# Kernel tuning notes

Measured on AMD Instinct MI355X. Metric: run time of the kernel, lower is better.

The kernel has to match this reference:

```python
import jax, jax.numpy as jnp
import numpy as np

L = 8      # number of history layers backsubstituted (history[2:] in the torch code)
D = 2048   # layer width


def setup_inputs() -> dict:
    key = jax.random.key(0)
    ks = jax.random.split(key, 8)
    lower = jax.random.normal(ks[6], (D,), dtype=jnp.float32)
    upper = lower + jax.random.uniform(ks[7], (D,), dtype=jnp.float32)  # ensure lower <= upper
    return {
        "A": jax.random.normal(ks[0], (D, D), dtype=jnp.float32) * 0.05,
        "b": jax.random.normal(ks[1], (D,), dtype=jnp.float32) * 0.05,
        "hist_Al": jax.random.normal(ks[2], (L, D, D), dtype=jnp.float32) * 0.05,
        "hist_Au": jax.random.normal(ks[3], (L, D, D), dtype=jnp.float32) * 0.05,
        "hist_bl": jax.random.normal(ks[4], (L, D), dtype=jnp.float32) * 0.05,
        "hist_bu": jax.random.normal(ks[5], (L, D), dtype=jnp.float32) * 0.05,
        "lower_in": lower,
        "upper_in": upper,
    }


def reference(A, b, hist_Al, hist_Au, hist_bl, hist_bu, lower_in, upper_in):
    # Affine layer sets Al = Au = A, bl = bu = b, then backsubstitutes
    # through the history in reverse order (torch loop: i = len-1 .. 2).
    def step(carry, dp):
        Al, Au, bl, bu = carry
        dAl, dAu, dbl, dbu = dp
        Al_pos = jnp.maximum(Al, 0.0)
        Al_neg = jnp.minimum(Al, 0.0)
        Au_pos = jnp.maximum(Au, 0.0)
        Au_neg = jnp.minimum(Au, 0.0)
        new_Al = Al_pos @ dAl + Al_neg @ dAu
        new_bl = Al_pos @ dbl + Al_neg @ dbu + bl
        new_Au = Au_pos @ dAu + Au_neg @ dAl
        new_bu = Au_pos @ dbu + Au_neg @ dbl + bu
        return (new_Al, new_Au, new_bl, new_bu), None

    init = (A, A, b, b)
    # reverse the history so scan walks from the last layer back to the first
    dps = (hist_Al[::-1], hist_Au[::-1], hist_bl[::-1], hist_bu[::-1])
    (Al, Au, bl, bu), _ = jax.lax.scan(step, init, dps)

    # final concretization against the input box (history[1] in the torch code)
    lower = jnp.maximum(Al, 0.0) @ lower_in + jnp.minimum(Al, 0.0) @ upper_in + bl
    upper = jnp.maximum(Au, 0.0) @ upper_in + jnp.minimum(Au, 0.0) @ lower_in + bu
    return lower, upper
```

## Files before the change

kernel.cpp:

```cpp
#include <hip/hip_runtime.h>
#include <cstdint>
#include <cstddef>

#define D 2048
#define L 8
#define KT 4096
#define BM 256
#define BN 128
#define BK 32
#define NT (KT / BK)
#define BUFSZ ((BM + BN) * BK)

typedef _Float16 f16;
typedef _Float16 f16x4 __attribute__((ext_vector_type(4)));
typedef _Float16 f16x8 __attribute__((ext_vector_type(8)));
typedef float f32x4 __attribute__((ext_vector_type(4)));

__device__ __forceinline__ void gload16(const void* g, void* l) {
  __builtin_amdgcn_global_load_lds(
      (const __attribute__((address_space(1))) void*)g,
      (__attribute__((address_space(3))) void*)l, 16, 0, 0);
}

__global__ __launch_bounds__(256) void k_init(
    const float* __restrict__ A, const float* __restrict__ b,
    const float* __restrict__ db1, const float* __restrict__ db2,
    f16* __restrict__ Ab, float* __restrict__ blbu, float* __restrict__ outacc) {
  const int m = blockIdx.x, tid = threadIdx.x;
  if (m < 2) {
    f32x4 z = {0.f, 0.f, 0.f, 0.f};
    *(f32x4*)(outacc + m * 2048 + tid * 8) = z;
    *(f32x4*)(outacc + m * 2048 + tid * 8 + 4) = z;
  }
  const int k = tid * 8;
  size_t i = (size_t)m * D + k;
  f32x4 a0 = *(const f32x4*)(A + i);
  f32x4 a1 = *(const f32x4*)(A + i + 4);
  f16x8 p, n;
  float cL = 0.f, cU = 0.f;
#pragma unroll
  for (int j = 0; j < 8; ++j) {
    float v = (j < 4) ? a0[j] : a1[j - 4];
    float pf = fmaxf(v, 0.f), nf = fminf(v, 0.f);
    p[j] = (f16)pf; n[j] = (f16)nf;
    float w1 = db1[k + j], w2 = db2[k + j];
    cL += pf * w1 + nf * w2;
    cU += pf * w2 + nf * w1;
  }
  size_t lo = (size_t)m * KT + k;
  size_t hi = (size_t)(D + m) * KT + k;
  *(f16x8*)(Ab + lo) = p;      *(f16x8*)(Ab + lo + D) = n;
  *(f16x8*)(Ab + hi) = n;      *(f16x8*)(Ab + hi + D) = p;

  __shared__ float redL[4], redU[4];
#pragma unroll
  for (int off = 32; off > 0; off >>= 1) {
    cL += __shfl_down(cL, off);
    cU += __shfl_down(cU, off);
  }
  const int wave = tid >> 6, lane = tid & 63;
  if (lane == 0) { redL[wave] = cL; redU[wave] = cU; }
  __syncthreads();
  if (tid == 0) {
    float bL = b[m] + redL[0] + redL[1] + redL[2] + redL[3];
    float bU = b[m] + redU[0] + redU[1] + redU[2] + redU[3];
    blbu[m] = bL; blbu[D + m] = bU;
  }
}

__device__ __forceinline__ void transpose_panel(
    const float* __restrict__ srcAl, const float* __restrict__ srcAu,
    f16* __restrict__ Bb, int blk, int tid) {
  const int z = blk >> 10;
  const int rem = blk & 1023;
  const float* src = z ? srcAu : srcAl;
  const int koff = z ? D : 0;
  const int nb = (rem & 31) * 64;
  const int kb = (rem >> 5) * 64;
  const int col = nb + (tid & 63);
  const int k0 = kb + (tid >> 6) * 16;
  float v[16];
#pragma unroll
  for (int j = 0; j < 16; ++j)
    v[j] = src[(size_t)(k0 + j) * D + col];
  f16x8 h0, h1;
#pragma unroll
  for (int j = 0; j < 8; ++j) { h0[j] = (f16)v[j]; h1[j] = (f16)v[8 + j]; }
  f16* dst = Bb + (size_t)col * KT + koff + k0;
  *(f16x8*)dst = h0;
  *(f16x8*)(dst + 8) = h1;
}

__global__ __launch_bounds__(256) void k_prep(
    const float* __restrict__ srcAl, const float* __restrict__ srcAu,
    f16* __restrict__ Bb) {
  transpose_panel(srcAl, srcAu, Bb, blockIdx.x, threadIdx.x);
}

__global__ __launch_bounds__(256, 2) void k_gemm(
    const f16* __restrict__ A,
    const f16* __restrict__ BT,
    f16* __restrict__ BTn,
    const float* __restrict__ nAl, const float* __restrict__ nAu,
    const float* __restrict__ w1, const float* __restrict__ w2,
    float* __restrict__ bdst,
    f16* __restrict__ An) {
  __shared__ __align__(16) f16 lds[3 * BUFSZ];

  if (blockIdx.x >= 256) {
    transpose_panel(nAl, nAu, BTn, blockIdx.x - 256, threadIdx.x);
    return;
  }

  const int flat = blockIdx.x;
  const int xcd = flat & 7, idx = flat >> 3;
  const int by = (xcd >> 1) * 4 + (idx >> 3);
  const int bx = (xcd & 1) * 8 + (idx & 7);
  const int m0 = by * BM;
  const int n0 = bx * BN;

  const int tid = threadIdx.x;
  const int wave = tid >> 6, lane = tid & 63;
  const int wm = (wave >> 1) * 128, wn = (wave & 1) * 64;
  const int lr = lane & 15, lq = lane >> 4;
  const int srow = lane >> 2;
  const int scol = ((lane & 3) ^ ((lane >> 3) & 3)) * 8;
  const int rchunk = (lq ^ ((lr >> 1) & 3)) * 8;

  f32x4 acc[8][4];
#pragma unroll
  for (int m = 0; m < 8; ++m)
#pragma unroll
    for (int n = 0; n < 4; ++n)
      acc[m][n] = (f32x4){0.f, 0.f, 0.f, 0.f};

  auto stage = [&](int kt, int buf) {
    f16* bA = lds + buf * BUFSZ;
    f16* bB = bA + BM * BK;
    const size_t gk = (size_t)kt * BK;
#pragma unroll
    for (int i = 0; i < 4; ++i) {
      const int r = i * 4 + wave;
      gload16(A + (size_t)(m0 + r * 16 + srow) * KT + gk + scol, bA + r * 512);
    }
#pragma unroll
    for (int i = 0; i < 2; ++i) {
      const int r = i * 4 + wave;
      gload16(BT + (size_t)(n0 + r * 16 + srow) * KT + gk + scol, bB + r * 512);
    }
  };

  stage(0, 0);
  stage(1, 1);
  asm volatile("s_waitcnt vmcnt(6)" ::: "memory");
  __builtin_amdgcn_sched_barrier(0);
  __builtin_amdgcn_s_barrier();
  __builtin_amdgcn_sched_barrier(0);

  for (int t = 0; t < NT; ++t) {
    const f16* bA = lds + (t % 3) * BUFSZ;
    const f16* bB = bA + BM * BK;
    if (t + 2 < NT) stage(t + 2, (t + 2) % 3);
    f16x8 af[8], bf[4];
#pragma unroll
    for (int m = 0; m < 8; ++m)
      af[m] = *(const f16x8*)(bA + (wm + m * 16 + lr) * BK + rchunk);
#pragma unroll
    for (int n = 0; n < 4; ++n)
      bf[n] = *(const f16x8*)(bB + (wn + n * 16 + lr) * BK + rchunk);
    __builtin_amdgcn_s_setprio(1);
#pragma unroll
    for (int m = 0; m < 8; ++m)
#pragma unroll
      for (int n = 0; n < 4; ++n)
        acc[m][n] = __builtin_amdgcn_mfma_f32_16x16x32_f16(
            bf[n], af[m], acc[m][n], 0, 0, 0);
    __builtin_amdgcn_s_setprio(0);
    if (t + 2 < NT) {
      asm volatile("s_waitcnt vmcnt(6)" ::: "memory");
    } else if (t + 1 < NT) {
      asm volatile("s_waitcnt vmcnt(0)" ::: "memory");
    }
    __builtin_amdgcn_sched_barrier(0);
    __builtin_amdgcn_s_barrier();
    __builtin_amdgcn_sched_barrier(0);
  }

  const int low = (m0 < D) ? 1 : 0;
  f32x4 w1v[4], w2v[4];
#pragma unroll
  for (int n = 0; n < 4; ++n) {
    const int col = n0 + wn + n * 16 + lq * 4;
    w1v[n] = *(const f32x4*)(w1 + col);
    w2v[n] = *(const f32x4*)(w2 + col);
  }
  float rowsum[8] = {0.f, 0.f, 0.f, 0.f, 0.f, 0.f, 0.f, 0.f};
#pragma unroll
  for (int m = 0; m < 8; ++m) {
#pragma unroll
    for (int n = 0; n < 4; ++n) {
      const size_t row = (size_t)(m0 + wm + m * 16 + lr);
      const int col = n0 + wn + n * 16 + lq * 4;
      f16x4 p, q;
#pragma unroll
      for (int r = 0; r < 4; ++r) {
        float v = acc[m][n][r];
        float pf = fmaxf(v, 0.f), qf = fminf(v, 0.f);
        p[r] = (f16)pf;
        q[r] = (f16)qf;
        float wa = low ? w1v[n][r] : w2v[n][r];
        float wb = low ? w2v[n][r] : w1v[n][r];
        rowsum[m] += pf * wa + qf * wb;
      }
      f16* base = An + row * KT + col;
      if (low) { *(f16x4*)base = p; *(f16x4*)(base + D) = q; }
      else     { *(f16x4*)base = q; *(f16x4*)(base + D) = p; }
    }
  }
#pragma unroll
  for (int m = 0; m < 8; ++m) {
    float v = rowsum[m];
    v += __shfl_down(v, 32);
    v += __shfl_down(v, 16);
    if (lane < 16)
      atomicAdd(bdst + m0 + wm + m * 16 + lane, v);
  }
}

__global__ __launch_bounds__(256) void k_final(
    const float* __restrict__ outacc, const float* __restrict__ blbu,
    float* __restrict__ out) {
  const int R = blockIdx.x * 256 + threadIdx.x;
  out[R] = outacc[R] + blbu[R];
}

extern "C" void kernel_launch(void* const* d_in, const int* in_sizes, int n_in,
                              void* d_out, int out_size, void* d_ws, size_t ws_size,
                              hipStream_t stream) {
  (void)in_sizes; (void)n_in; (void)out_size;
  const float* A   = (const float*)d_in[0];
  const float* b   = (const float*)d_in[1];
  const float* hAl = (const float*)d_in[2];
  const float* hAu = (const float*)d_in[3];
  const float* hbl = (const float*)d_in[4];
  const float* hbu = (const float*)d_in[5];
  const float* lo  = (const float*)d_in[6];
  const float* up  = (const float*)d_in[7];
  float* out = (float*)d_out;

  const size_t AS = (size_t)2 * D * KT;
  const size_t BS = (size_t)D * KT;
  const size_t MS = (size_t)D * D;
  char* base = (char*)d_ws;
  f16* Ab0   = (f16*)base;
  f16* Ab1   = Ab0 + AS;
  f16* Bb0   = Ab1 + AS;
  float* blbu   = (float*)(Bb0 + BS);
  float* outacc = blbu + 2 * D;
  f16* Bb1   = (f16*)(outacc + 2 * D);
  const size_t need_fused = (size_t)((char*)(Bb1 + BS) - base);
  const bool fused = ws_size >= need_fused;

  k_init<<<dim3(D), 256, 0, stream>>>(
      A, b, hbl + (size_t)7 * D, hbu + (size_t)7 * D, Ab0, blbu, outacc);
  k_prep<<<dim3(2048), 256, 0, stream>>>(
      hAl + (size_t)7 * MS, hAu + (size_t)7 * MS, Bb0);

  f16* cur = Ab0;
  f16* nxt = Ab1;
  for (int t = 0; t < L; ++t) {
    const int nlayer = 6 - t;
    const float* w1 = (t < 7) ? hbl + (size_t)nlayer * D : lo;
    const float* w2 = (t < 7) ? hbu + (size_t)nlayer * D : up;
    float* bd = (t < 7) ? blbu : outacc;
    f16* BT  = (fused && (t & 1)) ? Bb1 : Bb0;
    f16* BTn = fused ? ((t & 1) ? Bb0 : Bb1) : Bb0;
    const float* nl = (t < 7) ? hAl + (size_t)nlayer * MS : hAl;
    const float* nu = (t < 7) ? hAu + (size_t)nlayer * MS : hAu;
    if (!fused && t > 0)
      k_prep<<<dim3(2048), 256, 0, stream>>>(
          hAl + (size_t)(7 - t) * MS, hAu + (size_t)(7 - t) * MS, Bb0);
    const unsigned grid = (fused && t < 7) ? 2304u : 256u;
    k_gemm<<<dim3(grid), 256, 0, stream>>>(cur, BT, BTn, nl, nu, w1, w2, bd, nxt);
    f16* tmp = cur; cur = nxt; nxt = tmp;
  }
  k_final<<<dim3(2 * D / 256), 256, 0, stream>>>(outacc, blbu, out);
}
```

Measured before the change: 726.8 us.

## Use 8 waves per GEMM block with ping-pong interleaved loads and MFMA

Doubles the GEMM block to 512 threads (8 waves), so each wave owns a 64x64 tile instead of 128x64, which halves the per-wave accumulator registers. The K-step is split into two halves, each with its own barrier, so that LDS reads and global prefetch issue overlap with MFMA bursts from other waves. The transpose panel is rewritten for 512 threads, each handling 8 k-values. This risks more barrier overhead and lower occupancy per CU because of the larger blocks.

```diff
diff --git a/kernel.cpp b/kernel.cpp
--- a/kernel.cpp
+++ b/kernel.cpp
@@ -78,26 +78,24 @@
   const int nb = (rem & 31) * 64;
   const int kb = (rem >> 5) * 64;
   const int col = nb + (tid & 63);
-  const int k0 = kb + (tid >> 6) * 16;
-  float v[16];
-#pragma unroll
-  for (int j = 0; j < 16; ++j)
+  const int k0 = kb + (tid >> 6) * 8;
+  float v[8];
+#pragma unroll
+  for (int j = 0; j < 8; ++j)
     v[j] = src[(size_t)(k0 + j) * D + col];
-  f16x8 h0, h1;
-#pragma unroll
-  for (int j = 0; j < 8; ++j) { h0[j] = (f16)v[j]; h1[j] = (f16)v[8 + j]; }
-  f16* dst = Bb + (size_t)col * KT + koff + k0;
-  *(f16x8*)dst = h0;
-  *(f16x8*)(dst + 8) = h1;
-}
-
-__global__ __launch_bounds__(256) void k_prep(
+  f16x8 h;
+#pragma unroll
+  for (int j = 0; j < 8; ++j) h[j] = (f16)v[j];
+  *(f16x8*)(Bb + (size_t)col * KT + koff + k0) = h;
+}
+
+__global__ __launch_bounds__(512) void k_prep(
     const float* __restrict__ srcAl, const float* __restrict__ srcAu,
     f16* __restrict__ Bb) {
   transpose_panel(srcAl, srcAu, Bb, blockIdx.x, threadIdx.x);
 }
 
-__global__ __launch_bounds__(256, 2) void k_gemm(
+__global__ __launch_bounds__(512, 2) void k_gemm(
     const f16* __restrict__ A,
     const f16* __restrict__ BT,
     f16* __restrict__ BTn,
@@ -121,38 +119,47 @@
 
   const int tid = threadIdx.x;
   const int wave = tid >> 6, lane = tid & 63;
-  const int wm = (wave >> 1) * 128, wn = (wave & 1) * 64;
+  const int wm = (wave & 3) * 64, wn = (wave >> 2) * 64;
   const int lr = lane & 15, lq = lane >> 4;
   const int srow = lane >> 2;
   const int scol = ((lane & 3) ^ ((lane >> 3) & 3)) * 8;
   const int rchunk = (lq ^ ((lr >> 1) & 3)) * 8;
 
-  f32x4 acc[8][4];
-#pragma unroll
-  for (int m = 0; m < 8; ++m)
+  f32x4 acc[4][4];
+#pragma unroll
+  for (int m = 0; m < 4; ++m)
 #pragma unroll
     for (int n = 0; n < 4; ++n)
       acc[m][n] = (f32x4){0.f, 0.f, 0.f, 0.f};
 
-  auto stage = [&](int kt, int buf) {
-    f16* bA = lds + buf * BUFSZ;
-    f16* bB = bA + BM * BK;
-    const size_t gk = (size_t)kt * BK;
-#pragma unroll
-    for (int i = 0; i < 4; ++i) {
-      const int r = i * 4 + wave;
-      gload16(A + (size_t)(m0 + r * 16 + srow) * KT + gk + scol, bA + r * 512);
-    }
-#pragma unroll
-    for (int i = 0; i < 2; ++i) {
-      const int r = i * 4 + wave;
-      gload16(BT + (size_t)(n0 + r * 16 + srow) * KT + gk + scol, bB + r * 512);
-    }
+  auto stageA = [&](size_t gk, f16* sA, int i) {
+    const int r = i * 8 + wave;
+    gload16(A + (size_t)(m0 + r * 16 + srow) * KT + gk + scol, sA + r * 512);
   };
-
-  stage(0, 0);
-  stage(1, 1);
-  asm volatile("s_waitcnt vmcnt(6)" ::: "memory");
+  auto stageB = [&](size_t gk, f16* sB) {
+    gload16(BT + (size_t)(n0 + wave * 16 + srow) * KT + gk + scol,
+            sB + wave * 512);
+  };
+  auto lda = [&](const f16* bA, int m) {
+    return *(const f16x8*)(bA + (wm + m * 16 + lr) * BK + rchunk);
+  };
+  auto ldb = [&](const f16* bB, int n) {
+    return *(const f16x8*)(bB + (wn + n * 16 + lr) * BK + rchunk);
+  };
+
+#define SYNC_PRE()  do { __builtin_amdgcn_sched_barrier(0);                 \
+    __builtin_amdgcn_s_barrier();                                           \
+    asm volatile("s_waitcnt lgkmcnt(0)" ::: "memory");                      \
+    __builtin_amdgcn_sched_barrier(0); } while (0)
+#define SYNC_POST() do { __builtin_amdgcn_sched_barrier(0);                 \
+    __builtin_amdgcn_s_barrier(); } while (0)
+
+  { f16* s0 = lds;            f16* s0b = s0 + BM * BK;
+    f16* s1 = lds + BUFSZ;    f16* s1b = s1 + BM * BK;
+    stageA(0, s0, 0); stageA(0, s0, 1); stageB(0, s0b);
+    stageA(BK, s1, 0); stageA(BK, s1, 1); stageB(BK, s1b);
+  }
+  asm volatile("s_waitcnt vmcnt(3)" ::: "memory");
   __builtin_amdgcn_sched_barrier(0);
   __builtin_amdgcn_s_barrier();
   __builtin_amdgcn_sched_barrier(0);
@@ -160,30 +167,46 @@
   for (int t = 0; t < NT; ++t) {
     const f16* bA = lds + (t % 3) * BUFSZ;
     const f16* bB = bA + BM * BK;
-    if (t + 2 < NT) stage(t + 2, (t + 2) % 3);
-    f16x8 af[8], bf[4];
-#pragma unroll
-    for (int m = 0; m < 8; ++m)
-      af[m] = *(const f16x8*)(bA + (wm + m * 16 + lr) * BK + rchunk);
-#pragma unroll
-    for (int n = 0; n < 4; ++n)
-      bf[n] = *(const f16x8*)(bB + (wn + n * 16 + lr) * BK + rchunk);
+    f16* sA = lds + ((t + 2) % 3) * BUFSZ;
+    f16* sB = sA + BM * BK;
+    const bool pf = (t + 2 < NT);
+    const size_t gk = (size_t)(t + 2) * BK;
+
+    f16x8 b0 = ldb(bB, 0), b1 = ldb(bB, 1), b2 = ldb(bB, 2), b3 = ldb(bB, 3);
+    f16x8 a0 = lda(bA, 0), a1 = lda(bA, 1);
+    if (pf) { stageA(gk, sA, 0); stageA(gk, sA, 1); }
+    SYNC_PRE();
     __builtin_amdgcn_s_setprio(1);
-#pragma unroll
-    for (int m = 0; m < 8; ++m)
-#pragma unroll
-      for (int n = 0; n < 4; ++n)
-        acc[m][n] = __builtin_amdgcn_mfma_f32_16x16x32_f16(
-            bf[n], af[m], acc[m][n], 0, 0, 0);
+    acc[0][0] = __builtin_amdgcn_mfma_f32_16x16x32_f16(b0, a0, acc[0][0], 0, 0, 0);
+    acc[0][1] = __builtin_amdgcn_mfma_f32_16x16x32_f16(b1, a0, acc[0][1], 0, 0, 0);
+    acc[0][2] = __builtin_amdgcn_mfma_f32_16x16x32_f16(b2, a0, acc[0][2], 0, 0, 0);
+    acc[0][3] = __builtin_amdgcn_mfma_f32_16x16x32_f16(b3, a0, acc[0][3], 0, 0, 0);
+    acc[1][0] = __builtin_amdgcn_mfma_f32_16x16x32_f16(b0, a1, acc[1][0], 0, 0, 0);
+    acc[1][1] = __builtin_amdgcn_mfma_f32_16x16x32_f16(b1, a1, acc[1][1], 0, 0, 0);
+    acc[1][2] = __builtin_amdgcn_mfma_f32_16x16x32_f16(b2, a1, acc[1][2], 0, 0, 0);
+    acc[1][3] = __builtin_amdgcn_mfma_f32_16x16x32_f16(b3, a1, acc[1][3], 0, 0, 0);
     __builtin_amdgcn_s_setprio(0);
-    if (t + 2 < NT) {
-      asm volatile("s_waitcnt vmcnt(6)" ::: "memory");
+    SYNC_POST();
+
+    f16x8 a2 = lda(bA, 2), a3 = lda(bA, 3);
+    if (pf) {
+      stageB(gk, sB);
+      asm volatile("s_waitcnt vmcnt(3)" ::: "memory");
     } else if (t + 1 < NT) {
       asm volatile("s_waitcnt vmcnt(0)" ::: "memory");
     }
-    __builtin_amdgcn_sched_barrier(0);
-    __builtin_amdgcn_s_barrier();
-    __builtin_amdgcn_sched_barrier(0);
+    SYNC_PRE();
+    __builtin_amdgcn_s_setprio(1);
+    acc[2][0] = __builtin_amdgcn_mfma_f32_16x16x32_f16(b0, a2, acc[2][0], 0, 0, 0);
+    acc[2][1] = __builtin_amdgcn_mfma_f32_16x16x32_f16(b1, a2, acc[2][1], 0, 0, 0);
+    acc[2][2] = __builtin_amdgcn_mfma_f32_16x16x32_f16(b2, a2, acc[2][2], 0, 0, 0);
+    acc[2][3] = __builtin_amdgcn_mfma_f32_16x16x32_f16(b3, a2, acc[2][3], 0, 0, 0);
+    acc[3][0] = __builtin_amdgcn_mfma_f32_16x16x32_f16(b0, a3, acc[3][0], 0, 0, 0);
+    acc[3][1] = __builtin_amdgcn_mfma_f32_16x16x32_f16(b1, a3, acc[3][1], 0, 0, 0);
+    acc[3][2] = __builtin_amdgcn_mfma_f32_16x16x32_f16(b2, a3, acc[3][2], 0, 0, 0);
+    acc[3][3] = __builtin_amdgcn_mfma_f32_16x16x32_f16(b3, a3, acc[3][3], 0, 0, 0);
+    __builtin_amdgcn_s_setprio(0);
+    SYNC_POST();
   }
 
   const int low = (m0 < D) ? 1 : 0;
@@ -194,9 +217,9 @@
     w1v[n] = *(const f32x4*)(w1 + col);
     w2v[n] = *(const f32x4*)(w2 + col);
   }
-  float rowsum[8] = {0.f, 0.f, 0.f, 0.f, 0.f, 0.f, 0.f, 0.f};
-#pragma unroll
-  for (int m = 0; m < 8; ++m) {
+  float rowsum[4] = {0.f, 0.f, 0.f, 0.f};
+#pragma unroll
+  for (int m = 0; m < 4; ++m) {
 #pragma unroll
     for (int n = 0; n < 4; ++n) {
       const size_t row = (size_t)(m0 + wm + m * 16 + lr);
@@ -205,12 +228,12 @@
 #pragma unroll
       for (int r = 0; r < 4; ++r) {
         float v = acc[m][n][r];
-        float pf = fmaxf(v, 0.f), qf = fminf(v, 0.f);
-        p[r] = (f16)pf;
+        float pf2 = fmaxf(v, 0.f), qf = fminf(v, 0.f);
+        p[r] = (f16)pf2;
         q[r] = (f16)qf;
         float wa = low ? w1v[n][r] : w2v[n][r];
         float wb = low ? w2v[n][r] : w1v[n][r];
-        rowsum[m] += pf * wa + qf * wb;
+        rowsum[m] += pf2 * wa + qf * wb;
       }
       f16* base = An + row * KT + col;
       if (low) { *(f16x4*)base = p; *(f16x4*)(base + D) = q; }
@@ -218,7 +241,7 @@
     }
   }
 #pragma unroll
-  for (int m = 0; m < 8; ++m) {
+  for (int m = 0; m < 4; ++m) {
     float v = rowsum[m];
     v += __shfl_down(v, 32);
     v += __shfl_down(v, 16);
@@ -263,7 +286,7 @@
 
   k_init<<<dim3(D), 256, 0, stream>>>(
       A, b, hbl + (size_t)7 * D, hbu + (size_t)7 * D, Ab0, blbu, outacc);
-  k_prep<<<dim3(2048), 256, 0, stream>>>(
+  k_prep<<<dim3(2048), 512, 0, stream>>>(
       hAl + (size_t)7 * MS, hAu + (size_t)7 * MS, Bb0);
 
   f16* cur = Ab0;
@@ -278,10 +301,10 @@
     const float* nl = (t < 7) ? hAl + (size_t)nlayer * MS : hAl;
     const float* nu = (t < 7) ? hAu + (size_t)nlayer * MS : hAu;
     if (!fused && t > 0)
-      k_prep<<<dim3(2048), 256, 0, stream>>>(
+      k_prep<<<dim3(2048), 512, 0, stream>>>(
           hAl + (size_t)(7 - t) * MS, hAu + (size_t)(7 - t) * MS, Bb0);
     const unsigned grid = (fused && t < 7) ? 2304u : 256u;
-    k_gemm<<<dim3(grid), 256, 0, stream>>>(cur, BT, BTn, nl, nu, w1, w2, bd, nxt);
+    k_gemm<<<dim3(grid), 512, 0, stream>>>(cur, BT, BTn, nl, nu, w1, w2, bd, nxt);
     f16* tmp = cur; cur = nxt; nxt = tmp;
   }
   k_final<<<dim3(2 * D / 256), 256, 0, stream>>>(outacc, blbu, out);
```

Result: slower. 766.4 us (+5.5%).
